# Performance work log

Measured on AMD Instinct MI355X. Metric: run time of the kernel, lower is better.

The kernel has to match this reference:

```python
import jax, jax.numpy as jnp
import numpy as np

HEADS = 6
WIN = 7
DIM_IN = 192
DIM_OUT = 192
EPS = 1e-5


def _rel_pos_idx(w):
    # Faithful reproduction of Swin relative-position index construction.
    coords = np.stack(np.meshgrid(np.arange(w), np.arange(w), indexing='ij'))  # [2,w,w]
    flat = coords.reshape(2, -1)                                               # [2,N]
    rel = (flat[:, :, None] - flat[:, None, :]).transpose(1, 2, 0)             # [N,N,2]
    rel[..., 0] += w - 1
    rel[..., 1] += w - 1
    rel[..., 0] *= 2 * w - 1
    return rel.sum(-1)                                                         # [N,N]


def setup_inputs() -> dict:
    key = jax.random.key(0)
    ks = jax.random.split(key, 8)
    B, C, H, W = 32, DIM_IN, 56, 56
    D = DIM_OUT
    nW = (H // WIN) * (W // WIN)
    N = WIN * WIN
    return {
        'x': jax.random.normal(ks[0], (B, C, H, W), jnp.float32),
        'mask': jax.random.normal(ks[1], (nW, N, N), jnp.float32),
        'dw_w': jax.random.normal(ks[2], (C, 1, 3, 3), jnp.float32) * 0.05,
        'bn_gamma': jnp.ones((C,), jnp.float32),
        'bn_beta': jnp.zeros((C,), jnp.float32),
        'bn_mean': jnp.zeros((C,), jnp.float32),
        'bn_var': jnp.ones((C,), jnp.float32),
        'pw_w': jax.random.normal(ks[3], (3 * D, C), jnp.float32) * 0.02,
        'pw_b': jnp.zeros((3 * D,), jnp.float32),
        'proj_w': jax.random.normal(ks[4], (C, D), jnp.float32) * 0.02,
        'proj_b': jnp.zeros((C,), jnp.float32),
        'rel_bias_table': jax.random.normal(ks[5], ((2 * WIN - 1) ** 2, HEADS), jnp.float32) * 0.02,
    }


def reference(x, mask, dw_w, bn_gamma, bn_beta, bn_mean, bn_var, pw_w, pw_b, proj_w, proj_b, rel_bias_table):
    B, C, H, W = x.shape
    h, w = HEADS, WIN
    D = proj_w.shape[1]
    d = D // h
    sx, sy = H // w, W // w  # H,W divisible by window -> pad branch is a no-op
    N = w * w
    scale = D ** -0.5  # note: original scales by dim_out**-0.5, not head_dim

    # qkv = pointwise(bn(depthwise(x)))
    y = jax.lax.conv_general_dilated(
        x, dw_w, window_strides=(1, 1), padding=((1, 1), (1, 1)),
        feature_group_count=C, dimension_numbers=('NCHW', 'OIHW', 'NCHW'))
    inv = bn_gamma / jnp.sqrt(bn_var + EPS)
    y = (y - bn_mean[:, None, None]) * inv[:, None, None] + bn_beta[:, None, None]
    qkv = jnp.einsum('bchw,oc->bohw', y, pw_w) + pw_b[:, None, None]
    q, k, v = jnp.split(qkv, 3, axis=1)

    def to_win(t):  # b (h d) (sx w) (sy w) -> (b sx sy) h (w w) d
        t = t.reshape(B, h, d, sx, w, sy, w)
        return t.transpose(0, 3, 5, 1, 4, 6, 2).reshape(B * sx * sy, h, N, d)

    q, k, v = map(to_win, (q, k, v))

    dots = jnp.einsum('bhid,bhjd->bhij', q, k) * scale  # [B*nW, h, N, N]
    idx = jnp.asarray(_rel_pos_idx(w).reshape(-1))
    bias = rel_bias_table[idx].reshape(N, N, h).transpose(2, 0, 1)  # [h,N,N]
    dots = dots + bias[None]
    nW = mask.shape[0]
    dots = dots.reshape(B, nW, h, N, N) + mask[None, :, None]
    attn = jax.nn.softmax(dots.reshape(B * nW, h, N, N), axis=-1)

    out = jnp.einsum('bhij,bhjd->bhid', attn, v)  # [B*nW, h, N, d]
    out = out.reshape(B, sx, sy, h, w, w, d).transpose(0, 3, 6, 1, 4, 2, 5).reshape(B, D, H, W)
    return jnp.einsum('bchw,oc->bohw', out, proj_w) + proj_b[:, None, None]
```

## Files before the change

kernel.cpp:

```cpp
#include <hip/hip_runtime.h>


typedef __attribute__((ext_vector_type(8))) short bf16x8;
typedef __attribute__((ext_vector_type(4))) float f32x4;
typedef unsigned int uint32;

__device__ __forceinline__ unsigned short f2b(float f) {
    union { float f; unsigned u; } v; v.f = f;
    unsigned r = v.u + 0x7FFFu + ((v.u >> 16) & 1u);
    return (unsigned short)(r >> 16);
}

__device__ __forceinline__ void gload_lds16(const void* g, void* l) {
    __builtin_amdgcn_global_load_lds(
        (const __attribute__((address_space(1))) uint32*)g,
        (__attribute__((address_space(3))) uint32*)l, 16, 0, 0);
}

__global__ __launch_bounds__(256)
void k0_convert(const float* __restrict__ pw_w, const float* __restrict__ proj_w,
                unsigned* __restrict__ wq, unsigned* __restrict__ wp)
{
    int i = blockIdx.x * 256 + threadIdx.x;
    if (i < 55296) {
        float2 v = *(const float2*)(pw_w + 2 * i);
        wq[i] = (unsigned)f2b(v.x) | ((unsigned)f2b(v.y) << 16);
    } else {
        int j = i - 55296;
        float2 v = *(const float2*)(proj_w + 2 * j);
        wp[j] = (unsigned)f2b(v.x) | ((unsigned)f2b(v.y) << 16);
    }
}

#define K1S 61
__global__ __launch_bounds__(256)
void k1_dwconv(const float* __restrict__ x, const float* __restrict__ dw_w,
               const float* __restrict__ bn_gamma, const float* __restrict__ bn_beta,
               const float* __restrict__ bn_mean, const float* __restrict__ bn_var,
               unsigned* __restrict__ y)
{
    __shared__ float xs[64 * 3 * K1S];
    const int t = threadIdx.x;
    const int b = blockIdx.x / 56, r = blockIdx.x - (blockIdx.x / 56) * 56;
    const int cp = t & 31, cl0 = 2 * cp;

    for (int ch = 0; ch < 3; ++ch) {
        const int c0 = ch * 64;
        for (int it = 0; it < 11; ++it) {
            int item = t + 256 * it;
            if (item < 2688) {
                int cl = item / 42, rem = item - cl * 42;
                int rr = rem / 14, i4 = rem - rr * 14;
                int r2 = r + rr - 1;
                float4 v = make_float4(0.f, 0.f, 0.f, 0.f);
                if ((unsigned)r2 < 56u)
                    v = *(const float4*)(x + ((b * 192 + c0 + cl) * 56 + r2) * 56 + 4 * i4);
                float* dst = &xs[(cl * 3 + rr) * K1S + 1 + 4 * i4];
                dst[0] = v.x; dst[1] = v.y; dst[2] = v.z; dst[3] = v.w;
            }
        }
        if (t < 192) {
            int cl = t / 3, rr = t - (t / 3) * 3;
            xs[(cl * 3 + rr) * K1S + 0] = 0.f;
            xs[(cl * 3 + rr) * K1S + 57] = 0.f;
        }
        __syncthreads();
        const int cA = c0 + cl0, cB = cA + 1;
        float invA = bn_gamma[cA] * rsqrtf(bn_var[cA] + 1e-5f);
        float shA  = bn_beta[cA] - bn_mean[cA] * invA;
        float invB = bn_gamma[cB] * rsqrtf(bn_var[cB] + 1e-5f);
        float shB  = bn_beta[cB] - bn_mean[cB] * invB;
        float wA[9], wB[9];
#pragma unroll
        for (int q = 0; q < 9; ++q) { wA[q] = dw_w[cA * 9 + q]; wB[q] = dw_w[cB * 9 + q]; }
        const float* xa = &xs[(cl0 * 3) * K1S];
        const float* xb = &xs[((cl0 + 1) * 3) * K1S];
        for (int it = 0; it < 7; ++it) {
            int cc = (t >> 5) + 8 * it;
            float a0 = 0.f, a1 = 0.f;
#pragma unroll
            for (int dr = 0; dr < 3; ++dr)
#pragma unroll
                for (int dc = 0; dc < 3; ++dc) {
                    a0 += xa[dr * K1S + cc + dc] * wA[dr * 3 + dc];
                    a1 += xb[dr * K1S + cc + dc] * wB[dr * 3 + dc];
                }
            float y0 = a0 * invA + shA, y1 = a1 * invB + shB;
            int p = b * 3136 + r * 56 + cc;
            y[p * 96 + 32 * ch + cp] = (unsigned)f2b(y0) | ((unsigned)f2b(y1) << 16);
        }
        __syncthreads();
    }
}

__global__ __launch_bounds__(512, 4)
void k2_qkv(const char* __restrict__ yb, const char* __restrict__ wqb,
            const float* __restrict__ pw_b, char* __restrict__ qkvb)
{
    __shared__ __align__(16) char lds[73728];
    int bid = blockIdx.x;
    bid = (bid & 7) * 294 + (bid >> 3);
    const int pt = bid / 3, og = bid - (bid / 3) * 3;
    const int p0 = pt * 128;
    const int t = threadIdx.x, lane = t & 63, w = t >> 6;
    const int col = lane & 15, kg = lane >> 4;

    auto stageB = [&](int ot) {
        const char* gB = wqb + (size_t)(ot * 64) * 384;
#pragma unroll
        for (int it = 0; it < 3; ++it) {
            int dl = it * 8192 + w * 1024 + lane * 16;
            int i = dl / 384, c = dl - i * 384;
            gload_lds16(gB + i * 384 + (c ^ ((i & 7) << 4)), lds + 49152 + dl);
        }
    };
    {
        const char* gA = yb + (size_t)p0 * 384;
#pragma unroll
        for (int it = 0; it < 6; ++it) {
            int dl = it * 8192 + w * 1024 + lane * 16;
            int i = dl / 384, c = dl - i * 384;
            gload_lds16(gA + i * 384 + (c ^ ((i & 7) << 4)), lds + dl);
        }
        stageB(og * 3);
    }
    __syncthreads();

    const int wp = w & 3, wo = w >> 2;
    const f32x4 zz = {0.f, 0.f, 0.f, 0.f};
    for (int k = 0; k < 3; ++k) {
        const int ot = og * 3 + k;
        f32x4 acc[2][2];
        acc[0][0] = zz; acc[0][1] = zz; acc[1][0] = zz; acc[1][1] = zz;
#pragma unroll
        for (int kk = 0; kk < 6; ++kk) {
            const int c = 16 * kg + 64 * kk;
            bf16x8 a[2], bb[2];
#pragma unroll
            for (int mt = 0; mt < 2; ++mt) {
                int row = 32 * wp + 16 * mt + col;
                a[mt] = *(const bf16x8*)(lds + row * 384 + (c ^ ((row & 7) << 4)));
            }
#pragma unroll
            for (int nt = 0; nt < 2; ++nt) {
                int row = 32 * wo + 16 * nt + col;
                bb[nt] = *(const bf16x8*)(lds + 49152 + row * 384 + (c ^ ((row & 7) << 4)));
            }
#pragma unroll
            for (int mt = 0; mt < 2; ++mt)
#pragma unroll
                for (int nt = 0; nt < 2; ++nt)
                    acc[mt][nt] = __builtin_amdgcn_mfma_f32_16x16x32_bf16(a[mt], bb[nt], acc[mt][nt], 0, 0, 0);
        }
#pragma unroll
        for (int nt = 0; nt < 2; ++nt) {
            int o_g = ot * 64 + 32 * wo + 16 * nt + col;
            float pb = pw_b[o_g];
#pragma unroll
            for (int mt = 0; mt < 2; ++mt)
#pragma unroll
                for (int reg = 0; reg < 4; ++reg) {
                    int p_g = p0 + 32 * wp + 16 * mt + 4 * kg + reg;
                    *(unsigned short*)(qkvb + ((size_t)p_g * 576 + o_g) * 2) =
                        f2b(acc[mt][nt][reg] + pb);
                }
        }
        if (k < 2) {
            __syncthreads();
            stageB(ot + 1);
            __syncthreads();
        }
    }
}

#define QB3    0
#define KB3    19600
#define VTB3   39200
#define EB3    63776
#define DOTS3  70832
#define RS3    81024
#define K3LDS  81220
__global__ __launch_bounds__(512, 4)
void k3_attn(const char* __restrict__ qkvb, const float* __restrict__ mask,
             const float* __restrict__ rel_table, char* __restrict__ attb)
{
    __shared__ __align__(16) char lds[K3LDS];
    const int t = threadIdx.x, lane = t & 63, w = t >> 6;
    const int col = lane & 15, kg = lane >> 4;
    const int b = blockIdx.x >> 6, wid = blockIdx.x & 63;
    const int X0 = (wid >> 3) * 7, Y0 = (wid & 7) * 7;
    const float scale = 0.07216878364870323f;

    auto PIX = [&](int n) { int rr = n / 7; return b * 3136 + (X0 + rr) * 56 + Y0 + (n - rr * 7); };

#pragma unroll
    for (int it = 0; it < 3; ++it) {
        int item = t + 512 * it;
        if (item < 1176) {
            int r = item / 24, c8 = item - r * 24;
            size_t gb = (size_t)PIX(r) * 1152 + 16 * c8;
            *(bf16x8*)(lds + QB3 + r * 400 + 16 * c8) = *(const bf16x8*)(qkvb + gb);
            *(bf16x8*)(lds + KB3 + r * 400 + 16 * c8) = *(const bf16x8*)(qkvb + gb + 384);
        }
    }
#pragma unroll
    for (int it = 0; it < 3; ++it) {
        int item = t + 512 * it;
        if (item < 1176) {
            int j = item / 24, dd8 = item - j * 24;
            bf16x8 v = *(const bf16x8*)(qkvb + (size_t)PIX(j) * 1152 + 768 + 16 * dd8);
            int sw = (dd8 & 7) << 4;
#pragma unroll
            for (int i = 0; i < 8; ++i)
                *(unsigned short*)(lds + VTB3 + (8 * dd8 + i) * 128 + ((2 * j) ^ sw)) =
                    (unsigned short)v[i];
        }
    }
#pragma unroll
    for (int it = 0; it < 6; ++it) {
        int item = t + 512 * it;
        if (item < 2880) {
            int row = item / 15, jz = 49 + (item - (item / 15) * 15);
            *(unsigned short*)(lds + VTB3 + row * 128 + ((2 * jz) ^ (((row >> 3) & 7) << 4))) = 0;
        }
    }
    __syncthreads();

    const int jt = w & 3, ih = w >> 2;
    const int dd0 = 16 * (w & 1), i0p = 16 * (w >> 1);
    const f32x4 zz = {0.f, 0.f, 0.f, 0.f};

    for (int h = 0; h < 6; ++h) {
        {
            const int j0 = 16 * jt;
            bf16x8 a = *(const bf16x8*)(lds + KB3 + (j0 + col) * 400 + 64 * h + 16 * kg);
#pragma unroll
            for (int q = 0; q < 2; ++q) {
                int i0 = 32 * ih + 16 * q;
                bf16x8 bb = *(const bf16x8*)(lds + QB3 + (i0 + col) * 400 + 64 * h + 16 * kg);
                f32x4 d4 = __builtin_amdgcn_mfma_f32_16x16x32_bf16(a, bb, zz, 0, 0, 0);
                int i = i0 + col, jb = j0 + 4 * kg;
                if (i < 49 && jb <= 48)
                    *(f32x4*)(lds + DOTS3 + (i * 52 + jb) * 4) = d4;
            }
        }
        __syncthreads();
        if (t < 392) {
            int r = t >> 3, j8 = t & 7;
            float* drow = (float*)(lds + DOTS3) + r * 52;
            int ar = r / 7, br = r - ar * 7;
            const float* mrow = mask + wid * 2401 + r * 49;
            float mx = -3.4e38f;
            for (int j = j8; j < 49; j += 8) {
                int aj = j / 7, bj = j - aj * 7;
                float val = drow[j] * scale
                          + rel_table[((ar - aj + 6) * 13 + (br - bj + 6)) * 6 + h]
                          + mrow[j];
                drow[j] = val;
                mx = fmaxf(mx, val);
            }
            mx = fmaxf(mx, __shfl_xor(mx, 1));
            mx = fmaxf(mx, __shfl_xor(mx, 2));
            mx = fmaxf(mx, __shfl_xor(mx, 4));
            float s = 0.f;
            for (int j = j8; j < 49; j += 8) {
                float e = __expf(drow[j] - mx);
                s += e;
                *(unsigned short*)(lds + EB3 + r * 144 + 2 * j) = f2b(e);
            }
            *(unsigned short*)(lds + EB3 + r * 144 + 2 * (49 + j8)) = 0;
            if (57 + j8 < 64)
                *(unsigned short*)(lds + EB3 + r * 144 + 2 * (57 + j8)) = 0;
            s += __shfl_xor(s, 1);
            s += __shfl_xor(s, 2);
            s += __shfl_xor(s, 4);
            if (j8 == 0) ((float*)(lds + RS3))[r] = 1.f / s;
        }
        __syncthreads();
        {
            f32x4 acc = zz;
            const int ddg = h * 32 + dd0 + col;
#pragma unroll
            for (int kk = 0; kk < 2; ++kk) {
                bf16x8 a = *(const bf16x8*)(lds + VTB3 + ddg * 128 +
                               ((16 * kg + 64 * kk) ^ (((ddg >> 3) & 7) << 4)));
                bf16x8 bb = *(const bf16x8*)(lds + EB3 + (i0p + col) * 144 + 16 * kg + 64 * kk);
                acc = __builtin_amdgcn_mfma_f32_16x16x32_bf16(a, bb, acc, 0, 0, 0);
            }
            int i = i0p + col;
            if (i < 49) {
                float rs = ((const float*)(lds + RS3))[i];
                unsigned u0 = (unsigned)f2b(acc[0] * rs) | ((unsigned)f2b(acc[1] * rs) << 16);
                unsigned u1 = (unsigned)f2b(acc[2] * rs) | ((unsigned)f2b(acc[3] * rs) << 16);
                *(uint2*)(attb + ((size_t)PIX(i) * 192 + h * 32 + dd0 + 4 * kg) * 2) =
                    make_uint2(u0, u1);
            }
        }
    }
}

__global__ __launch_bounds__(512, 4)
void k4_proj(const char* __restrict__ attb, const char* __restrict__ wpb,
             const float* __restrict__ proj_b, float* __restrict__ outp)
{
    __shared__ __align__(16) char lds[73728];
    int bid = blockIdx.x;
    bid = (bid & 7) * 294 + (bid >> 3);
    const int pt = bid / 3, ot = bid - (bid / 3) * 3;
    const int p0 = pt * 128, o0 = ot * 64;
    const int t = threadIdx.x, lane = t & 63, w = t >> 6;
    const int col = lane & 15, kg = lane >> 4;

    {
        const char* gW = wpb + (size_t)o0 * 384;
        const char* gX = attb + (size_t)p0 * 384;
#pragma unroll
        for (int it = 0; it < 9; ++it) {
            int d = it * 8192 + w * 1024 + lane * 16;
            int dl = (it < 3) ? d : d - 24576;
            const char* gb = (it < 3) ? gW : gX;
            int i = dl / 384, c = dl - i * 384;
            gload_lds16(gb + i * 384 + (c ^ ((i & 7) << 4)), lds + d);
        }
    }
    __syncthreads();

    const int wo = w & 1, wp4 = w >> 1;
    const f32x4 zz = {0.f, 0.f, 0.f, 0.f};
    f32x4 acc[2][2];
    acc[0][0] = zz; acc[0][1] = zz; acc[1][0] = zz; acc[1][1] = zz;
#pragma unroll
    for (int kk = 0; kk < 6; ++kk) {
        const int c = 16 * kg + 64 * kk;
        bf16x8 a[2], bb[2];
#pragma unroll
        for (int mt = 0; mt < 2; ++mt) {
            int row = 32 * wo + 16 * mt + col;
            a[mt] = *(const bf16x8*)(lds + row * 384 + (c ^ ((row & 7) << 4)));
        }
#pragma unroll
        for (int nt = 0; nt < 2; ++nt) {
            int row = 32 * wp4 + 16 * nt + col;
            bb[nt] = *(const bf16x8*)(lds + 24576 + row * 384 + (c ^ ((row & 7) << 4)));
        }
#pragma unroll
        for (int mt = 0; mt < 2; ++mt)
#pragma unroll
            for (int nt = 0; nt < 2; ++nt)
                acc[mt][nt] = __builtin_amdgcn_mfma_f32_16x16x32_bf16(a[mt], bb[nt], acc[mt][nt], 0, 0, 0);
    }
#pragma unroll
    for (int nt = 0; nt < 2; ++nt) {
        int p_g = p0 + 32 * wp4 + 16 * nt + col;
        int bg = p_g / 3136, hw = p_g - bg * 3136;
#pragma unroll
        for (int mt = 0; mt < 2; ++mt)
#pragma unroll
            for (int reg = 0; reg < 4; ++reg) {
                int o_g = o0 + 32 * wo + 16 * mt + 4 * kg + reg;
                outp[(size_t)(bg * 192 + o_g) * 3136 + hw] = acc[mt][nt][reg] + proj_b[o_g];
            }
    }
}

#define TPB 512
#define OT_B   0
#define YT_B   20800
#define WA_B   41600
#define QS_B   54400
#define KS_B   58560
#define VT_B   62720
#define E_B    67328
#define LDS_TOTAL 76480
#define DOTS_B WA_B
#define RS_B   (WA_B + 10192)
#define XS_B   WA_B
#define DWL_B  OT_B
#define SC_B   (OT_B + 3456)
#define SH_B   (OT_B + 4224)

__global__ __launch_bounds__(TPB, 4)
void swin_mfma_kernel(const float* __restrict__ x,
                      const float* __restrict__ mask,
                      const float* __restrict__ dw_w,
                      const float* __restrict__ bn_gamma,
                      const float* __restrict__ bn_beta,
                      const float* __restrict__ bn_mean,
                      const float* __restrict__ bn_var,
                      const float* __restrict__ pw_w,
                      const float* __restrict__ pw_b,
                      const float* __restrict__ proj_w,
                      const float* __restrict__ proj_b,
                      const float* __restrict__ rel_table,
                      float* __restrict__ out)
{
    __shared__ __align__(16) char lds[LDS_TOTAL];
    const int t    = threadIdx.x;
    const int blk  = blockIdx.x;
    const int b    = blk >> 6;
    const int wid  = blk & 63;
    const int X0   = (wid >> 3) * 7, Y0 = (wid & 7) * 7;
    const int lane = t & 63;
    const int w    = t >> 6;
    const int col  = lane & 15;
    const int kg   = lane >> 4;
    const float scale = 0.07216878364870323f;

    if (t < 192) {
        float inv = bn_gamma[t] * rsqrtf(bn_var[t] + 1e-5f);
        ((float*)(lds + SC_B))[t] = inv;
        ((float*)(lds + SH_B))[t] = bn_beta[t] - bn_mean[t] * inv;
    }
    for (int half = 0; half < 2; ++half) {
        const int c0 = half * 96;
        for (int idx = t; idx < 96 * 9; idx += TPB)
            ((float*)(lds + DWL_B))[idx] = dw_w[c0 * 9 + idx];
        for (int idx = t; idx < 96 * 81; idx += TPB) {
            int cl = idx / 81, p = idx - cl * 81;
            int di = p / 9, dj = p - di * 9;
            int r = X0 - 1 + di, cc = Y0 - 1 + dj;
            float v = 0.f;
            if ((unsigned)r < 56u && (unsigned)cc < 56u)
                v = x[((b * 192 + c0 + cl) * 56 + r) * 56 + cc];
            ((float*)(lds + XS_B))[cl * 84 + p] = v;
        }
        __syncthreads();
        for (int idx = t; idx < 96 * 49; idx += TPB) {
            int cl = idx / 49, n = idx - cl * 49;
            int i = n / 7, j = n - i * 7;
            const float* xc = (const float*)(lds + XS_B) + cl * 84;
            const float* wl = (const float*)(lds + DWL_B) + cl * 9;
            float acc = 0.f;
#pragma unroll
            for (int dr = 0; dr < 3; ++dr)
#pragma unroll
                for (int ds = 0; ds < 3; ++ds)
                    acc += xc[(i + dr) * 9 + (j + ds)] * wl[dr * 3 + ds];
            int c = c0 + cl;
            float yv = acc * ((float*)(lds + SC_B))[c] + ((float*)(lds + SH_B))[c];
            *(unsigned short*)(lds + YT_B + n * 400 + c * 2) = f2b(yv);
        }
        __syncthreads();
    }
    const int o_l = 16 * (w & 1);
    const int n0g = 16 * (w >> 1);
    for (int h = 0; h < 6; ++h) {
#pragma unroll 1
        for (int m = 0; m < 3; ++m) {
            const int o_base = m * 192 + h * 32;
            const float* src = pw_w + o_base * 192;
            for (int idx = t; idx < 3072; idx += TPB) {
                int ol = idx / 96, c2 = idx - ol * 96;
                float2 v = *(const float2*)(src + ol * 192 + c2 * 2);
                unsigned p = ((unsigned)f2b(v.y) << 16) | (unsigned)f2b(v.x);
                *(unsigned*)(lds + WA_B + ol * 400 + c2 * 4) = p;
            }
            __syncthreads();
            {
                f32x4 acc = {0.f, 0.f, 0.f, 0.f};
                const char* aP = lds + WA_B + (o_l + col) * 400 + 16 * kg;
                const char* bP = lds + YT_B + (n0g + col) * 400 + 16 * kg;
#pragma unroll
                for (int kk = 0; kk < 6; ++kk) {
                    bf16x8 a  = *(const bf16x8*)(aP + 64 * kk);
                    bf16x8 bb = *(const bf16x8*)(bP + 64 * kk);
                    acc = __builtin_amdgcn_mfma_f32_16x16x32_bf16(a, bb, acc, 0, 0, 0);
                }
                const int n = n0g + col;
#pragma unroll
                for (int reg = 0; reg < 4; ++reg) {
                    int od = o_l + 4 * kg + reg;
                    float val = acc[reg] + pw_b[o_base + od];
                    if (m == 2) {
                        *(unsigned short*)(lds + VT_B + od * 144 + n * 2) =
                            f2b(n < 49 ? val : 0.f);
                    } else if (n < 49) {
                        int dst = (m == 0 ? QS_B : KS_B);
                        *(unsigned short*)(lds + dst + n * 80 + od * 2) = f2b(val);
                    }
                }
            }
            __syncthreads();
        }
        {
            const int i0 = 16 * (w & 3);
            const int jp = w >> 2;
            bf16x8 a = *(const bf16x8*)(lds + QS_B + (i0 + col) * 80 + 16 * kg);
            f32x4 acc[2];
#pragma unroll
            for (int jt = 0; jt < 2; ++jt) {
                int j0 = 32 * jp + 16 * jt;
                bf16x8 bb = *(const bf16x8*)(lds + KS_B + (j0 + col) * 80 + 16 * kg);
                f32x4 z = {0.f, 0.f, 0.f, 0.f};
                acc[jt] = __builtin_amdgcn_mfma_f32_16x16x32_bf16(a, bb, z, 0, 0, 0);
            }
#pragma unroll
            for (int jt = 0; jt < 2; ++jt) {
                int j = 32 * jp + 16 * jt + col;
                if (j < 49) {
                    int aj = (j * 9363) >> 16, bj = j - aj * 7;
#pragma unroll
                    for (int reg = 0; reg < 4; ++reg) {
                        int i = i0 + 4 * kg + reg;
                        if (i < 49) {
                            int ai = (i * 9363) >> 16, bi = i - ai * 7;
                            int ridx = (ai - aj + 6) * 13 + (bi - bj + 6);
                            float val = acc[jt][reg] * scale
                                      + rel_table[ridx * 6 + h]
                                      + mask[wid * 2401 + i * 49 + j];
                            *(float*)(lds + DOTS_B + (i * 52 + j) * 4) = val;
                        }
                    }
                }
            }
        }
        __syncthreads();
        if (t < 392) {
            const int r = t >> 3, j8 = t & 7;
            const float* drow = (const float*)(lds + DOTS_B) + r * 52;
            float mx = -3.4e38f;
            for (int j = j8; j < 49; j += 8) mx = fmaxf(mx, drow[j]);
            mx = fmaxf(mx, __shfl_xor(mx, 1));
            mx = fmaxf(mx, __shfl_xor(mx, 2));
            mx = fmaxf(mx, __shfl_xor(mx, 4));
            float s = 0.f;
            for (int j = j8; j < 49; j += 8) {
                float e = __expf(drow[j] - mx);
                s += e;
                *(unsigned short*)(lds + E_B + r * 144 + j * 2) = f2b(e);
            }
            *(unsigned short*)(lds + E_B + r * 144 + (49 + j8) * 2) = 0;
            if (57 + j8 < 64)
                *(unsigned short*)(lds + E_B + r * 144 + (57 + j8) * 2) = 0;
            s += __shfl_xor(s, 1);
            s += __shfl_xor(s, 2);
            s += __shfl_xor(s, 4);
            if (j8 == 0) ((float*)(lds + RS_B))[r] = 1.f / s;
        }
        __syncthreads();
        {
            const int i0  = 16 * (w & 3);
            const int dd0 = 16 * (w >> 2);
            f32x4 acc = {0.f, 0.f, 0.f, 0.f};
#pragma unroll
            for (int kk = 0; kk < 2; ++kk) {
                bf16x8 a  = *(const bf16x8*)(lds + E_B  + (i0 + col) * 144 + 64 * kk + 16 * kg);
                bf16x8 bb = *(const bf16x8*)(lds + VT_B + (dd0 + col) * 144 + 64 * kk + 16 * kg);
                acc = __builtin_amdgcn_mfma_f32_16x16x32_bf16(a, bb, acc, 0, 0, 0);
            }
            const int dd = dd0 + col;
#pragma unroll
            for (int reg = 0; reg < 4; ++reg) {
                int i = i0 + 4 * kg + reg;
                if (i < 49) {
                    float val = acc[reg] * ((const float*)(lds + RS_B))[i];
                    *(unsigned short*)(lds + OT_B + i * 400 + (h * 32 + dd) * 2) = f2b(val);
                }
            }
        }
        __syncthreads();
    }
#pragma unroll 1
    for (int og = 0; og < 6; ++og) {
        const float* src = proj_w + og * 32 * 192;
        for (int idx = t; idx < 3072; idx += TPB) {
            int ol = idx / 96, c2 = idx - ol * 96;
            float2 v = *(const float2*)(src + ol * 192 + c2 * 2);
            unsigned p = ((unsigned)f2b(v.y) << 16) | (unsigned)f2b(v.x);
            *(unsigned*)(lds + WA_B + ol * 400 + c2 * 4) = p;
        }
        __syncthreads();
        {
            f32x4 acc = {0.f, 0.f, 0.f, 0.f};
            const char* aP = lds + WA_B + (o_l + col) * 400 + 16 * kg;
            const char* bP = lds + OT_B + (n0g + col) * 400 + 16 * kg;
#pragma unroll
            for (int kk = 0; kk < 6; ++kk) {
                bf16x8 a  = *(const bf16x8*)(aP + 64 * kk);
                bf16x8 bb = *(const bf16x8*)(bP + 64 * kk);
                acc = __builtin_amdgcn_mfma_f32_16x16x32_bf16(a, bb, acc, 0, 0, 0);
            }
            const int n = n0g + col;
            if (n < 49) {
                int i = n / 7, j = n - i * 7;
                long base = ((long)(b * 192) * 3136) + (X0 + i) * 56 + (Y0 + j);
#pragma unroll
                for (int reg = 0; reg < 4; ++reg) {
                    int o = og * 32 + o_l + 4 * kg + reg;
                    out[base + (long)o * 3136] = acc[reg] + proj_b[o];
                }
            }
        }
        __syncthreads();
    }
}

extern "C" void kernel_launch(void* const* d_in, const int* in_sizes, int n_in,
                              void* d_out, int out_size, void* d_ws, size_t ws_size,
                              hipStream_t stream) {
    const float* x         = (const float*)d_in[0];
    const float* mask      = (const float*)d_in[1];
    const float* dw_w      = (const float*)d_in[2];
    const float* bn_gamma  = (const float*)d_in[3];
    const float* bn_beta   = (const float*)d_in[4];
    const float* bn_mean   = (const float*)d_in[5];
    const float* bn_var    = (const float*)d_in[6];
    const float* pw_w      = (const float*)d_in[7];
    const float* pw_b      = (const float*)d_in[8];
    const float* proj_w    = (const float*)d_in[9];
    const float* proj_b    = (const float*)d_in[10];
    const float* rel_table = (const float*)d_in[11];
    float* outp            = (float*)d_out;

    const size_t NEED = 192970752ULL;
    if (ws_size >= NEED) {
        char* ws   = (char*)d_ws;
        char* y    = ws;
        char* qkv  = ws + 38535168;
        char* att  = ws + 154140672;
        char* wq   = ws + 192675840;
        char* wp   = ws + 192897024;

        hipLaunchKernelGGL(k0_convert, dim3(288), dim3(256), 0, stream,
                           pw_w, proj_w, (unsigned*)wq, (unsigned*)wp);
        hipLaunchKernelGGL(k1_dwconv, dim3(1792), dim3(256), 0, stream,
                           x, dw_w, bn_gamma, bn_beta, bn_mean, bn_var, (unsigned*)y);
        hipLaunchKernelGGL(k2_qkv, dim3(2352), dim3(512), 0, stream,
                           y, wq, pw_b, qkv);
        hipLaunchKernelGGL(k3_attn, dim3(2048), dim3(512), 0, stream,
                           qkv, mask, rel_table, att);
        hipLaunchKernelGGL(k4_proj, dim3(2352), dim3(512), 0, stream,
                           att, wp, proj_b, outp);
    } else {
        hipLaunchKernelGGL(swin_mfma_kernel, dim3(32 * 64), dim3(512), 0, stream,
                           x, mask, dw_w, bn_gamma, bn_beta, bn_mean, bn_var,
                           pw_w, pw_b, proj_w, proj_b, rel_table, outp);
    }
}
```

Baseline: 377.3 us.

## Split dwconv by channel groups, stage qkv output via LDS, fuse attention bias into MFMA epilogue

```diff
diff --git a/kernel.cpp b/kernel.cpp
--- a/kernel.cpp
+++ b/kernel.cpp
@@ -39,44 +39,50 @@
                const float* __restrict__ bn_mean, const float* __restrict__ bn_var,
                unsigned* __restrict__ y)
 {
-    __shared__ float xs[64 * 3 * K1S];
+    __shared__ float xs[32 * 3 * K1S];
     const int t = threadIdx.x;
-    const int b = blockIdx.x / 56, r = blockIdx.x - (blockIdx.x / 56) * 56;
-    const int cp = t & 31, cl0 = 2 * cp;
-
-    for (int ch = 0; ch < 3; ++ch) {
-        const int c0 = ch * 64;
-        for (int it = 0; it < 11; ++it) {
-            int item = t + 256 * it;
-            if (item < 2688) {
-                int cl = item / 42, rem = item - cl * 42;
-                int rr = rem / 14, i4 = rem - rr * 14;
-                int r2 = r + rr - 1;
-                float4 v = make_float4(0.f, 0.f, 0.f, 0.f);
-                if ((unsigned)r2 < 56u)
-                    v = *(const float4*)(x + ((b * 192 + c0 + cl) * 56 + r2) * 56 + 4 * i4);
-                float* dst = &xs[(cl * 3 + rr) * K1S + 1 + 4 * i4];
-                dst[0] = v.x; dst[1] = v.y; dst[2] = v.z; dst[3] = v.w;
-            }
-        }
-        if (t < 192) {
-            int cl = t / 3, rr = t - (t / 3) * 3;
-            xs[(cl * 3 + rr) * K1S + 0] = 0.f;
-            xs[(cl * 3 + rr) * K1S + 57] = 0.f;
-        }
-        __syncthreads();
-        const int cA = c0 + cl0, cB = cA + 1;
-        float invA = bn_gamma[cA] * rsqrtf(bn_var[cA] + 1e-5f);
-        float shA  = bn_beta[cA] - bn_mean[cA] * invA;
-        float invB = bn_gamma[cB] * rsqrtf(bn_var[cB] + 1e-5f);
-        float shB  = bn_beta[cB] - bn_mean[cB] * invB;
-        float wA[9], wB[9];
-#pragma unroll
-        for (int q = 0; q < 9; ++q) { wA[q] = dw_w[cA * 9 + q]; wB[q] = dw_w[cB * 9 + q]; }
-        const float* xa = &xs[(cl0 * 3) * K1S];
-        const float* xb = &xs[((cl0 + 1) * 3) * K1S];
-        for (int it = 0; it < 7; ++it) {
-            int cc = (t >> 5) + 8 * it;
+    const int bid = blockIdx.x;
+    const int b = bid / 336, rem = bid - b * 336;
+    const int r = rem / 6, g = rem - (rem / 6) * 6;
+    const int c0 = g * 32;
+
+#pragma unroll
+    for (int it = 0; it < 6; ++it) {
+        int item = t + 256 * it;
+        if (item < 1344) {
+            int cl = item / 42, rem2 = item - cl * 42;
+            int rr = rem2 / 14, i4 = rem2 - rr * 14;
+            int r2 = r + rr - 1;
+            float4 v = make_float4(0.f, 0.f, 0.f, 0.f);
+            if ((unsigned)r2 < 56u)
+                v = *(const float4*)(x + ((b * 192 + c0 + cl) * 56 + r2) * 56 + 4 * i4);
+            float* dst = &xs[(cl * 3 + rr) * K1S + 1 + 4 * i4];
+            dst[0] = v.x; dst[1] = v.y; dst[2] = v.z; dst[3] = v.w;
+        }
+    }
+    if (t < 192) {
+        int cl = t / 6, rem2 = t - cl * 6;
+        int rr = rem2 >> 1, side = rem2 & 1;
+        xs[(cl * 3 + rr) * K1S + (side ? 57 : 0)] = 0.f;
+    }
+    __syncthreads();
+
+    const int cp = t & 15;
+    const int ccq = t >> 4;
+    const int cA = c0 + 2 * cp, cB = cA + 1;
+    float invA = bn_gamma[cA] * rsqrtf(bn_var[cA] + 1e-5f);
+    float shA  = bn_beta[cA] - bn_mean[cA] * invA;
+    float invB = bn_gamma[cB] * rsqrtf(bn_var[cB] + 1e-5f);
+    float shB  = bn_beta[cB] - bn_mean[cB] * invB;
+    float wA[9], wB[9];
+#pragma unroll
+    for (int q = 0; q < 9; ++q) { wA[q] = dw_w[cA * 9 + q]; wB[q] = dw_w[cB * 9 + q]; }
+    const float* xa = &xs[(2 * cp) * 3 * K1S];
+    const float* xb = &xs[(2 * cp + 1) * 3 * K1S];
+#pragma unroll
+    for (int it = 0; it < 4; ++it) {
+        int cc = ccq + 16 * it;
+        if (cc < 56) {
             float a0 = 0.f, a1 = 0.f;
 #pragma unroll
             for (int dr = 0; dr < 3; ++dr)
@@ -87,9 +93,8 @@
                 }
             float y0 = a0 * invA + shA, y1 = a1 * invB + shB;
             int p = b * 3136 + r * 56 + cc;
-            y[p * 96 + 32 * ch + cp] = (unsigned)f2b(y0) | ((unsigned)f2b(y1) << 16);
-        }
-        __syncthreads();
+            y[p * 96 + 16 * g + cp] = (unsigned)f2b(y0) | ((unsigned)f2b(y1) << 16);
+        }
     }
 }
 
@@ -128,10 +133,16 @@
 
     const int wp = w & 3, wo = w >> 2;
     const f32x4 zz = {0.f, 0.f, 0.f, 0.f};
+    f32x4 acc3[3][2][2];
+#pragma unroll
     for (int k = 0; k < 3; ++k) {
-        const int ot = og * 3 + k;
-        f32x4 acc[2][2];
-        acc[0][0] = zz; acc[0][1] = zz; acc[1][0] = zz; acc[1][1] = zz;
+#pragma unroll
+        for (int mt = 0; mt < 2; ++mt)
+#pragma unroll
+            for (int nt = 0; nt < 2; ++nt) acc3[k][mt][nt] = zz;
+    }
+#pragma unroll
+    for (int k = 0; k < 3; ++k) {
 #pragma unroll
         for (int kk = 0; kk < 6; ++kk) {
             const int c = 16 * kg + 64 * kk;
@@ -150,26 +161,37 @@
             for (int mt = 0; mt < 2; ++mt)
 #pragma unroll
                 for (int nt = 0; nt < 2; ++nt)
-                    acc[mt][nt] = __builtin_amdgcn_mfma_f32_16x16x32_bf16(a[mt], bb[nt], acc[mt][nt], 0, 0, 0);
-        }
-#pragma unroll
-        for (int nt = 0; nt < 2; ++nt) {
-            int o_g = ot * 64 + 32 * wo + 16 * nt + col;
-            float pb = pw_b[o_g];
-#pragma unroll
-            for (int mt = 0; mt < 2; ++mt)
-#pragma unroll
-                for (int reg = 0; reg < 4; ++reg) {
-                    int p_g = p0 + 32 * wp + 16 * mt + 4 * kg + reg;
-                    *(unsigned short*)(qkvb + ((size_t)p_g * 576 + o_g) * 2) =
-                        f2b(acc[mt][nt][reg] + pb);
-                }
+                    acc3[k][mt][nt] = __builtin_amdgcn_mfma_f32_16x16x32_bf16(a[mt], bb[nt], acc3[k][mt][nt], 0, 0, 0);
         }
         if (k < 2) {
             __syncthreads();
-            stageB(ot + 1);
+            stageB(og * 3 + k + 1);
             __syncthreads();
         }
+    }
+    __syncthreads();
+#pragma unroll
+    for (int k = 0; k < 3; ++k)
+#pragma unroll
+        for (int nt = 0; nt < 2; ++nt) {
+            int o_l = k * 64 + 32 * wo + 16 * nt + col;
+            float pb = pw_b[og * 192 + o_l];
+#pragma unroll
+            for (int mt = 0; mt < 2; ++mt)
+#pragma unroll
+                for (int reg = 0; reg < 4; ++reg) {
+                    int p_l = 32 * wp + 16 * mt + 4 * kg + reg;
+                    *(unsigned short*)(lds + p_l * 384 +
+                        ((2 * o_l) ^ ((p_l & 7) << 4))) = f2b(acc3[k][mt][nt][reg] + pb);
+                }
+        }
+    __syncthreads();
+#pragma unroll
+    for (int it = 0; it < 6; ++it) {
+        int item = t + 512 * it;
+        int p = item / 24, c8 = item - p * 24;
+        bf16x8 v = *(const bf16x8*)(lds + p * 384 + ((16 * c8) ^ ((p & 7) << 4)));
+        *(bf16x8*)(qkvb + (size_t)(p0 + p) * 1152 + og * 384 + 16 * c8) = v;
     }
 }
 
@@ -230,35 +252,52 @@
     const int dd0 = 16 * (w & 1), i0p = 16 * (w >> 1);
     const f32x4 zz = {0.f, 0.f, 0.f, 0.f};
 
+    int iQ[2], aiQ[2], biQ[2];
+#pragma unroll
+    for (int q = 0; q < 2; ++q) {
+        int i = 32 * ih + 16 * q + col;
+        iQ[q] = i;
+        aiQ[q] = (i * 9363) >> 16;
+        biQ[q] = i - aiQ[q] * 7;
+    }
+    const int j0 = 16 * jt, jb = j0 + 4 * kg;
+
     for (int h = 0; h < 6; ++h) {
         {
-            const int j0 = 16 * jt;
             bf16x8 a = *(const bf16x8*)(lds + KB3 + (j0 + col) * 400 + 64 * h + 16 * kg);
 #pragma unroll
             for (int q = 0; q < 2; ++q) {
                 int i0 = 32 * ih + 16 * q;
                 bf16x8 bb = *(const bf16x8*)(lds + QB3 + (i0 + col) * 400 + 64 * h + 16 * kg);
                 f32x4 d4 = __builtin_amdgcn_mfma_f32_16x16x32_bf16(a, bb, zz, 0, 0, 0);
-                int i = i0 + col, jb = j0 + 4 * kg;
-                if (i < 49 && jb <= 48)
+                int i = iQ[q];
+                if (i < 49 && jb <= 48) {
+                    const float* mrow = mask + (wid * 49 + i) * 49;
+                    const int ai = aiQ[q], bi = biQ[q];
+                    if (jb < 48) {
+                        float4 mk = *(const float4*)(mrow + jb);
+#pragma unroll
+                        for (int reg = 0; reg < 4; ++reg) {
+                            int j = jb + reg;
+                            int aj = (j * 9363) >> 16, bj = j - aj * 7;
+                            int ridx = (ai - aj + 6) * 13 + (bi - bj + 6);
+                            d4[reg] = d4[reg] * scale + rel_table[ridx * 6 + h]
+                                    + (&mk.x)[reg];
+                        }
+                    } else {
+                        int ridx = ai * 13 + bi;
+                        d4[0] = d4[0] * scale + rel_table[ridx * 6 + h] + mrow[48];
+                    }
                     *(f32x4*)(lds + DOTS3 + (i * 52 + jb) * 4) = d4;
+                }
             }
         }
         __syncthreads();
         if (t < 392) {
             int r = t >> 3, j8 = t & 7;
-            float* drow = (float*)(lds + DOTS3) + r * 52;
-            int ar = r / 7, br = r - ar * 7;
-            const float* mrow = mask + wid * 2401 + r * 49;
+            const float* drow = (const float*)(lds + DOTS3) + r * 52;
             float mx = -3.4e38f;
-            for (int j = j8; j < 49; j += 8) {
-                int aj = j / 7, bj = j - aj * 7;
-                float val = drow[j] * scale
-                          + rel_table[((ar - aj + 6) * 13 + (br - bj + 6)) * 6 + h]
-                          + mrow[j];
-                drow[j] = val;
-                mx = fmaxf(mx, val);
-            }
+            for (int j = j8; j < 49; j += 8) mx = fmaxf(mx, drow[j]);
             mx = fmaxf(mx, __shfl_xor(mx, 1));
             mx = fmaxf(mx, __shfl_xor(mx, 2));
             mx = fmaxf(mx, __shfl_xor(mx, 4));
@@ -623,7 +662,7 @@
 
         hipLaunchKernelGGL(k0_convert, dim3(288), dim3(256), 0, stream,
                            pw_w, proj_w, (unsigned*)wq, (unsigned*)wp);
-        hipLaunchKernelGGL(k1_dwconv, dim3(1792), dim3(256), 0, stream,
+        hipLaunchKernelGGL(k1_dwconv, dim3(32 * 56 * 6), dim3(256), 0, stream,
                            x, dw_w, bn_gamma, bn_beta, bn_mean, bn_var, (unsigned*)y);
         hipLaunchKernelGGL(k2_qkv, dim3(2352), dim3(512), 0, stream,
                            y, wq, pw_b, qkv);
```

New measurement: 346.4 us. -8.2%, faster.
